# Optimization experiments

Measured on AMD Instinct MI355X. Metric: run time of the kernel, lower is better.

## Reference

```python
import jax, jax.numpy as jnp
import numpy as np

M, A, E, H = 2048, 64, 128, 256
NUM_BOND_TYPES, NUM_ATOM_TYPES = 4, 118

def setup_inputs() -> dict:
    key = jax.random.key(0)
    ks = jax.random.split(key, 12)
    s = 0.02
    return {
        'node_rep': jax.random.normal(ks[0], (M, A, H), jnp.float32),
        'edge_index': jax.random.randint(ks[1], (M, 2, E), 0, A, jnp.int32),
        'bond_type_target': jax.random.randint(ks[2], (M, E), 0, NUM_BOND_TYPES, jnp.int32),
        'atom_type_target': jax.random.randint(ks[3], (M, A), 0, NUM_ATOM_TYPES, jnp.int32),
        'Wp1': jax.random.normal(ks[4], (H, H), jnp.float32) * s, 'bp1': jnp.zeros((H,), jnp.float32),
        'Wp2': jax.random.normal(ks[5], (H, H), jnp.float32) * s, 'bp2': jnp.zeros((H,), jnp.float32),
        'Wb1': jax.random.normal(ks[6], (2 * H, H), jnp.float32) * s, 'bb1': jnp.zeros((H,), jnp.float32),
        'Wb2': jax.random.normal(ks[7], (H, NUM_BOND_TYPES), jnp.float32) * s, 'bb2': jnp.zeros((NUM_BOND_TYPES,), jnp.float32),
        'Wa1': jax.random.normal(ks[8], (H, H), jnp.float32) * s, 'ba1': jnp.zeros((H,), jnp.float32),
        'Wa2': jax.random.normal(ks[9], (H, NUM_ATOM_TYPES), jnp.float32) * s, 'ba2': jnp.zeros((NUM_ATOM_TYPES,), jnp.float32),
    }

def _mlp(x, W1, b1, W2, b2):
    return jnp.maximum(x @ W1 + b1, 0.0) @ W2 + b2

def reference(node_rep, edge_index, bond_type_target, atom_type_target,
              Wp1, bp1, Wp2, bp2, Wb1, bb1, Wb2, bb2, Wa1, ba1, Wa2, ba2):
    # bond_if_proj: per-atom 2-layer MLP (dropout=0 -> identity)  [M,A,H]
    proj = _mlp(node_rep, Wp1, bp1, Wp2, bp2)
    # gather bond endpoint reps: index_select over atoms per molecule  [M,E,H]
    start = jnp.take_along_axis(proj, edge_index[:, 0, :, None], axis=1)
    end = jnp.take_along_axis(proj, edge_index[:, 1, :, None], axis=1)
    bt_in = jnp.concatenate([start, end], axis=-1)            # [M,E,2H]
    bt_logits = _mlp(bt_in, Wb1, bb1, Wb2, bb2)               # [M,E,4]
    bt_logp = jax.nn.log_softmax(bt_logits, axis=-1)
    # per-molecule mean CE averaged over molecules == global mean (equal sizes)
    bond_type_loss = -jnp.mean(jnp.take_along_axis(bt_logp, bond_type_target[..., None], axis=-1))
    bond_type_acc = jnp.mean((jnp.argmax(bt_logits, axis=-1) == bond_type_target).astype(jnp.float32))
    # atom type classifier on raw node reps  [M,A,118]
    at_logits = _mlp(node_rep, Wa1, ba1, Wa2, ba2)
    at_logp = jax.nn.log_softmax(at_logits, axis=-1)
    atom_type_loss = -jnp.mean(jnp.take_along_axis(at_logp, atom_type_target[..., None], axis=-1))
    atom_type_acc = jnp.mean((jnp.argmax(at_logits, axis=-1) == atom_type_target).astype(jnp.float32))
    loss = 0.5 * bond_type_loss + 0.5 * atom_type_loss
    return loss, bond_type_acc, atom_type_acc
```

## Files before the change

kernel.cpp:

```cpp
#include <hip/hip_runtime.h>
#include <hip/hip_bf16.h>

typedef __bf16 bf16x8 __attribute__((ext_vector_type(8)));
typedef float f32x16 __attribute__((ext_vector_type(16)));

__device__ inline unsigned short f2bf(float f) {
  __hip_bfloat16 h = __float2bfloat16(f);
  return *reinterpret_cast<unsigned short*>(&h);
}
__device__ inline unsigned pack2bf(float a, float b) {
  return (unsigned)f2bf(a) | ((unsigned)f2bf(b) << 16);
}
__device__ inline uint2 pack4bf(float a, float b, float c, float d) {
  uint2 r; r.x = pack2bf(a, b); r.y = pack2bf(c, d); return r;
}
__device__ inline bf16x8 as_bf16x8(uint4 v) { return __builtin_bit_cast(bf16x8, v); }
__device__ inline float bitf(unsigned u) { return __builtin_bit_cast(float, u); }
__device__ inline f32x16 mfma16(bf16x8 a, bf16x8 b, f32x16 c) {
  return __builtin_amdgcn_mfma_f32_32x32x16_bf16(a, b, c, 0, 0, 0);
}

#define BR(XB, R, KK)                                                          \
  ((XB) + (((((R) * 32 + l31) << 9) + ((KK) << 5) + (h << 4)) ^ swz))

#define GEMMS(XB, WPTR)                                                        \
  {                                                                            \
    const unsigned char* wb_ = (const unsigned char*)(WPTR) +                  \
                               ((cw + l31) << 5) + (h << 4);                   \
    acc00 = zero; acc01 = zero; acc10 = zero; acc11 = zero;                    \
    bf16x8 pB0 = *(const bf16x8*)BR(XB, 0, 0);                                 \
    bf16x8 pB1 = *(const bf16x8*)BR(XB, 1, 0);                                 \
    uint4 pA0 = *(const uint4*)(wb_);                                          \
    uint4 pA1 = *(const uint4*)(wb_ + 1024);                                   \
    _Pragma("clang loop unroll(disable)")                                      \
    for (int kk = 0; kk < 16; kk += 2) {                                       \
      bf16x8 qB0 = *(const bf16x8*)BR(XB, 0, kk + 1);                          \
      bf16x8 qB1 = *(const bf16x8*)BR(XB, 1, kk + 1);                          \
      uint4 qA0 = *(const uint4*)(wb_ + ((kk + 1) << 13));                     \
      uint4 qA1 = *(const uint4*)(wb_ + ((kk + 1) << 13) + 1024);              \
      acc00 = mfma16(as_bf16x8(pA0), pB0, acc00);                              \
      acc10 = mfma16(as_bf16x8(pA1), pB0, acc10);                              \
      acc01 = mfma16(as_bf16x8(pA0), pB1, acc01);                              \
      acc11 = mfma16(as_bf16x8(pA1), pB1, acc11);                              \
      if (kk + 2 < 16) {                                                       \
        pB0 = *(const bf16x8*)BR(XB, 0, kk + 2);                               \
        pB1 = *(const bf16x8*)BR(XB, 1, kk + 2);                               \
        pA0 = *(const uint4*)(wb_ + ((kk + 2) << 13));                         \
        pA1 = *(const uint4*)(wb_ + ((kk + 2) << 13) + 1024);                  \
      }                                                                        \
      acc00 = mfma16(as_bf16x8(qA0), qB0, acc00);                              \
      acc10 = mfma16(as_bf16x8(qA1), qB0, acc10);                              \
      acc01 = mfma16(as_bf16x8(qA0), qB1, acc01);                              \
      acc11 = mfma16(as_bf16x8(qA1), qB1, acc11);                              \
    }                                                                          \
  }

#define WB22(DB, ACC, R, C, BIASPTR)                                           \
  _Pragma("unroll")                                                            \
  for (int g = 0; g < 4; ++g) {                                                \
    int xr_ = (R) * 32 + l31;                                                  \
    int col = cw + (C) * 32 + g * 8 + h * 4;                                   \
    float4 bb = *(const float4*)((BIASPTR) + col);                             \
    float v0_ = fmaxf(ACC[4 * g + 0] + bb.x, 0.f);                             \
    float v1_ = fmaxf(ACC[4 * g + 1] + bb.y, 0.f);                             \
    float v2_ = fmaxf(ACC[4 * g + 2] + bb.z, 0.f);                             \
    float v3_ = fmaxf(ACC[4 * g + 3] + bb.w, 0.f);                             \
    int off = ((xr_ << 9) + (col << 1)) ^ ((xr_ & 7) << 4);                    \
    *(uint2*)((DB) + off) = pack4bf(v0_, v1_, v2_, v3_);                       \
  }

#define WB22R(DB, ACC, R, C)                                                   \
  _Pragma("unroll")                                                            \
  for (int g = 0; g < 4; ++g) {                                                \
    int xr_ = (R) * 32 + l31;                                                  \
    int col = cw + (C) * 32 + g * 8 + h * 4;                                   \
    int off = ((xr_ << 9) + (col << 1)) ^ ((xr_ & 7) << 4);                    \
    *(uint2*)((DB) + off) = pack4bf(ACC[4 * g + 0], ACC[4 * g + 1],            \
                                    ACC[4 * g + 2], ACC[4 * g + 3]);           \
  }

#define STAGE_X(DST, SRC)                                                      \
  _Pragma("unroll")                                                            \
  for (int it = 0; it < 4; ++it) {                                             \
    int lb = (it * 512 + tid) * 16;                                            \
    int d_ = lb ^ (((lb >> 9) & 7) << 4);                                      \
    const float4* s4 = (const float4*)((SRC) + (lb >> 1));                     \
    float4 f0 = s4[0], f1 = s4[1];                                             \
    uint4 v_ = { pack2bf(f0.x, f0.y), pack2bf(f0.z, f0.w),                     \
                 pack2bf(f1.x, f1.y), pack2bf(f1.z, f1.w) };                   \
    *(uint4*)((DST) + d_) = v_;                                                \
  }

__global__ __launch_bounds__(256) void k_pack(
    const float* __restrict__ wp1, const float* __restrict__ wa1,
    const float* __restrict__ wa2,
    unsigned short* __restrict__ dp1, unsigned short* __restrict__ da1,
    unsigned short* __restrict__ da2, float* __restrict__ accum)
{
  int b = blockIdx.x, tid = threadIdx.x;
  if (b == 0 && tid < 8) accum[tid] = 0.f;
  const float* src; unsigned short* dst; int e, logN, Nreal;
  if (b < 256)       { src = wp1; dst = dp1; e = b * 256 + tid;          logN = 8; Nreal = 256; }
  else if (b < 512)  { src = wa1; dst = da1; e = (b - 256) * 256 + tid;  logN = 8; Nreal = 256; }
  else               { src = wa2; dst = da2; e = (b - 512) * 256 + tid;  logN = 7; Nreal = 118; }
  int dk = e & 15;
  int rest = e >> 4;
  int n = rest & ((1 << logN) - 1);
  int kk = rest >> logN;
  int k = kk * 16 + dk;
  float v = (n < Nreal) ? src[k * Nreal + n] : 0.f;
  dst[e] = f2bf(v);
}

__global__ __launch_bounds__(256) void k_fold(
    const float* __restrict__ wp2, const float* __restrict__ wb1,
    const float* __restrict__ bp2, const float* __restrict__ bb1,
    unsigned short* __restrict__ dct, unsigned short* __restrict__ dcb,
    float* __restrict__ bias_e)
{
  int b = blockIdx.x, n = threadIdx.x;
  if (b < 512) {
    int k = b & 255;
    int off = (b < 256) ? 0 : 256;
    float s = 0.f;
    for (int t = 0; t < 256; ++t)
      s += wp2[k * 256 + t] * wb1[(t + off) * 256 + n];
    unsigned short* dst = (b < 256) ? dct : dcb;
    dst[((k >> 4) * 256 + n) * 16 + (k & 15)] = f2bf(s);
  } else {
    float s = bb1[n];
    for (int t = 0; t < 256; ++t)
      s += bp2[t] * (wb1[t * 256 + n] + wb1[(256 + t) * 256 + n]);
    bias_e[n] = s;
  }
}

__global__ __launch_bounds__(512, 4) void k_mol(
    const float* __restrict__ node, const int* __restrict__ eidx,
    const int* __restrict__ btt, const int* __restrict__ att,
    const unsigned short* __restrict__ wp1p, const float* __restrict__ bp1,
    const unsigned short* __restrict__ wctp, const unsigned short* __restrict__ wcbp,
    const float* __restrict__ bias_e, const float* __restrict__ wb2,
    const float* __restrict__ bb2,
    const unsigned short* __restrict__ wa1p, const float* __restrict__ ba1,
    const unsigned short* __restrict__ wa2p, const float* __restrict__ ba2,
    float* __restrict__ accum)
{
  __shared__ __align__(16) unsigned char bufA[32768];
  __shared__ __align__(16) unsigned char bufB[32768];
  __shared__ float s_bias[256];
  __shared__ float4 s_wb2[256];
  __shared__ float s_b2a[128];
  __shared__ float s_red[16];
  const int tid = threadIdx.x;
  const int lane = tid & 63;
  const int w = tid >> 6;
  const int l31 = lane & 31;
  const int h = lane >> 5;
  const int swz = (l31 & 7) << 4;
  const int mat = w >> 2;
  const int cw = (w & 3) * 64;
  const int m = blockIdx.x;

  STAGE_X(bufA, node + (long)m * 16384);
  if (tid < 256) {
    s_bias[tid] = bias_e[tid];
    s_wb2[tid] = ((const float4*)wb2)[tid];
  }
  if (tid < 128) s_b2a[tid] = (tid < 118) ? ba2[tid] : 0.f;
  const int t_at = att[m * 64 + (tid >> 3)];
  __syncthreads();

  f32x16 zero = {};
  f32x16 acc00, acc01, acc10, acc11;

  GEMMS(bufA, mat ? wp1p : wa1p);
  if (mat == 0) {
    WB22(bufB, acc00, 0, 0, ba1);
    WB22(bufB, acc10, 0, 1, ba1);
    WB22(bufB, acc01, 1, 0, ba1);
    WB22(bufB, acc11, 1, 1, ba1);
  }
  __syncthreads();
  if (mat == 1) {
    WB22(bufA, acc00, 0, 0, bp1);
    WB22(bufA, acc10, 0, 1, bp1);
    WB22(bufA, acc01, 1, 0, bp1);
    WB22(bufA, acc11, 1, 1, bp1);
  }
  __syncthreads();

  f32x16 aL = zero;
  {
    const int cw2 = (w & 3) * 32;
    const int R2 = w >> 2;
    const unsigned char* wb_ = (const unsigned char*)wa2p +
                               ((cw2 + l31) << 5) + (h << 4);
    bf16x8 pB = *(const bf16x8*)BR(bufB, R2, 0);
    uint4 pA = *(const uint4*)(wb_);
    _Pragma("clang loop unroll(disable)")
    for (int kk = 0; kk < 16; kk += 2) {
      bf16x8 qB = *(const bf16x8*)BR(bufB, R2, kk + 1);
      uint4 qA = *(const uint4*)(wb_ + ((kk + 1) << 12));
      aL = mfma16(as_bf16x8(pA), pB, aL);
      if (kk + 2 < 16) {
        pB = *(const bf16x8*)BR(bufB, R2, kk + 2);
        pA = *(const uint4*)(wb_ + ((kk + 2) << 12));
      }
      aL = mfma16(as_bf16x8(qA), qB, aL);
    }
  }
  __syncthreads();

  {
    const int cw2 = (w & 3) * 32;
    const int r0 = (w >> 2) * 32 + l31;
    const int rx = (r0 & 7) << 4;
    #pragma unroll
    for (int g = 0; g < 4; ++g) {
      int colb = cw2 + 8 * g + 4 * h;
      uint4 val;
      val.x = __builtin_bit_cast(unsigned, aL[4 * g + 0] + s_b2a[colb + 0]);
      val.y = __builtin_bit_cast(unsigned, aL[4 * g + 1] + s_b2a[colb + 1]);
      val.z = __builtin_bit_cast(unsigned, aL[4 * g + 2] + s_b2a[colb + 2]);
      val.w = __builtin_bit_cast(unsigned, aL[4 * g + 3] + s_b2a[colb + 3]);
      *(uint4*)(bufB + (((r0 << 9) + (colb << 2)) ^ rx)) = val;
    }
  }
  __syncthreads();

  {
    const int row = tid >> 3, g8 = tid & 7;
    const unsigned char* lr = bufB + (row << 9);
    const int rx = (row & 7) << 4;
    float mx = -3.0e38f; int am = 127;
    #pragma unroll
    for (int j = 0; j < 4; ++j) {
      int ch = g8 + 8 * j;
      if (ch < 30) {
        float4 f = *(const float4*)(lr + (((ch << 4)) ^ rx));
        int c = ch * 4;
        if (f.x > mx) { mx = f.x; am = c; }
        if (f.y > mx) { mx = f.y; am = c + 1; }
        if (c + 2 < 118 && f.z > mx) { mx = f.z; am = c + 2; }
        if (c + 3 < 118 && f.w > mx) { mx = f.w; am = c + 3; }
      }
    }
    #pragma unroll
    for (int d = 1; d < 8; d <<= 1) {
      float mo = __shfl_xor(mx, d); int amo = __shfl_xor(am, d);
      if (mo > mx || (mo == mx && amo < am)) { mx = mo; am = amo; }
    }
    float s = 0.f, vt = 0.f;
    #pragma unroll
    for (int j = 0; j < 4; ++j) {
      int ch = g8 + 8 * j;
      if (ch < 30) {
        float4 f = *(const float4*)(lr + (((ch << 4)) ^ rx));
        int c = ch * 4;
        s += __expf(f.x - mx);
        s += __expf(f.y - mx);
        if (c + 2 < 118) s += __expf(f.z - mx);
        if (c + 3 < 118) s += __expf(f.w - mx);
        if (c == t_at) vt = f.x;
        if (c + 1 == t_at) vt = f.y;
        if (c + 2 == t_at) vt = f.z;
        if (c + 3 == t_at) vt = f.w;
      }
    }
    #pragma unroll
    for (int d = 1; d < 8; d <<= 1) { s += __shfl_xor(s, d); vt += __shfl_xor(vt, d); }
    float ce = 0.f, cc = 0.f;
    if (g8 == 0) { ce = __logf(s) + mx - vt; cc = (am == t_at) ? 1.f : 0.f; }
    #pragma unroll
    for (int d = 1; d < 64; d <<= 1) { ce += __shfl_xor(ce, d); cc += __shfl_xor(cc, d); }
    if (lane == 0) { s_red[w * 2] = ce; s_red[w * 2 + 1] = cc; }
  }

  GEMMS(bufA, mat ? wcbp : wctp);
  const int es = eidx[m * 256 + (tid >> 2)];
  const int ed = eidx[m * 256 + 128 + (tid >> 2)];
  const int etg = btt[m * 128 + (tid >> 2)];
  const float b20 = bb2[0], b21 = bb2[1], b22 = bb2[2], b23 = bb2[3];
  __syncthreads();
  if (tid == 0) {
    float sa = 0.f, sb = 0.f;
    #pragma unroll
    for (int i = 0; i < 8; ++i) { sa += s_red[2 * i]; sb += s_red[2 * i + 1]; }
    atomicAdd(accum + 2, sa);
    atomicAdd(accum + 3, sb);
  }
  if (mat == 0) {
    WB22R(bufA, acc00, 0, 0);
    WB22R(bufA, acc10, 0, 1);
    WB22R(bufA, acc01, 1, 0);
    WB22R(bufA, acc11, 1, 1);
  } else {
    WB22R(bufB, acc00, 0, 0);
    WB22R(bufB, acc10, 0, 1);
    WB22R(bufB, acc01, 1, 0);
    WB22R(bufB, acc11, 1, 1);
  }
  __syncthreads();

  {
    const int qf = tid & 3;
    float lg0 = 0.f, lg1 = 0.f, lg2 = 0.f, lg3 = 0.f;
    #pragma unroll
    for (int j = 0; j < 8; ++j) {
      int c0 = qf * 64 + j * 8;
      int offS = ((es << 9) + (c0 << 1)) ^ ((es & 7) << 4);
      int offD = ((ed << 9) + (c0 << 1)) ^ ((ed & 7) << 4);
      uint4 us = *(const uint4*)(bufA + offS);
      uint4 ud = *(const uint4*)(bufB + offD);
      const unsigned* pu = (const unsigned*)&us;
      const unsigned* pv = (const unsigned*)&ud;
      #pragma unroll
      for (int q = 0; q < 4; ++q) {
        unsigned ua = pu[q], ub = pv[q];
        int c = c0 + 2 * q;
        float hlo = bitf(ua << 16) + bitf(ub << 16) + s_bias[c];
        float hhi = bitf(ua & 0xffff0000u) + bitf(ub & 0xffff0000u) + s_bias[c + 1];
        hlo = fmaxf(hlo, 0.f); hhi = fmaxf(hhi, 0.f);
        float4 w0 = s_wb2[c], w1 = s_wb2[c + 1];
        lg0 = fmaf(hlo, w0.x, fmaf(hhi, w1.x, lg0));
        lg1 = fmaf(hlo, w0.y, fmaf(hhi, w1.y, lg1));
        lg2 = fmaf(hlo, w0.z, fmaf(hhi, w1.z, lg2));
        lg3 = fmaf(hlo, w0.w, fmaf(hhi, w1.w, lg3));
      }
    }
    lg0 += __shfl_xor(lg0, 1); lg1 += __shfl_xor(lg1, 1);
    lg2 += __shfl_xor(lg2, 1); lg3 += __shfl_xor(lg3, 1);
    lg0 += __shfl_xor(lg0, 2); lg1 += __shfl_xor(lg1, 2);
    lg2 += __shfl_xor(lg2, 2); lg3 += __shfl_xor(lg3, 2);
    float ce = 0.f, cc = 0.f;
    if (qf == 0) {
      float l0 = lg0 + b20, l1 = lg1 + b21, l2 = lg2 + b22, l3 = lg3 + b23;
      int t = etg;
      int am = 0; float mx = l0;
      if (l1 > mx) { mx = l1; am = 1; }
      if (l2 > mx) { mx = l2; am = 2; }
      if (l3 > mx) { mx = l3; am = 3; }
      float s = __expf(l0 - mx) + __expf(l1 - mx) + __expf(l2 - mx) + __expf(l3 - mx);
      float lt = (t == 0) ? l0 : (t == 1) ? l1 : (t == 2) ? l2 : l3;
      ce = __logf(s) + mx - lt;
      cc = (am == t) ? 1.f : 0.f;
    }
    #pragma unroll
    for (int d = 1; d < 64; d <<= 1) { ce += __shfl_xor(ce, d); cc += __shfl_xor(cc, d); }
    if (lane == 0) { s_red[w * 2] = ce; s_red[w * 2 + 1] = cc; }
    __syncthreads();
    if (tid == 0) {
      float sa = 0.f, sb = 0.f;
      #pragma unroll
      for (int i = 0; i < 8; ++i) { sa += s_red[2 * i]; sb += s_red[2 * i + 1]; }
      atomicAdd(accum + 0, sa);
      atomicAdd(accum + 1, sb);
    }
  }
}

__global__ __launch_bounds__(64) void k_final(const float* __restrict__ accum,
                                              float* __restrict__ out)
{
  if (threadIdx.x == 0) {
    float bce = accum[0] / 262144.f;
    float bcc = accum[1] / 262144.f;
    float ace = accum[2] / 131072.f;
    float acc_ = accum[3] / 131072.f;
    out[0] = 0.5f * bce + 0.5f * ace;
    out[1] = bcc;
    out[2] = acc_;
  }
}

extern "C" void kernel_launch(void* const* d_in, const int* in_sizes, int n_in,
                              void* d_out, int out_size, void* d_ws, size_t ws_size,
                              hipStream_t stream)
{
  const float* node = (const float*)d_in[0];
  const int* eidx   = (const int*)d_in[1];
  const int* btt    = (const int*)d_in[2];
  const int* att    = (const int*)d_in[3];
  const float* Wp1 = (const float*)d_in[4];
  const float* bp1 = (const float*)d_in[5];
  const float* Wp2 = (const float*)d_in[6];
  const float* bp2 = (const float*)d_in[7];
  const float* Wb1 = (const float*)d_in[8];
  const float* bb1 = (const float*)d_in[9];
  const float* Wb2 = (const float*)d_in[10];
  const float* bb2 = (const float*)d_in[11];
  const float* Wa1 = (const float*)d_in[12];
  const float* ba1 = (const float*)d_in[13];
  const float* Wa2 = (const float*)d_in[14];
  const float* ba2 = (const float*)d_in[15];

  char* ws = (char*)d_ws;
  float* accum = (float*)ws;
  unsigned short* dp1 = (unsigned short*)(ws + 256);
  unsigned short* da1 = (unsigned short*)(ws + 131328);
  unsigned short* da2 = (unsigned short*)(ws + 262400);
  unsigned short* dct = (unsigned short*)(ws + 327936);
  unsigned short* dcb = (unsigned short*)(ws + 459008);
  float* bias_e       = (float*)(ws + 590080);

  k_pack<<<640, 256, 0, stream>>>(Wp1, Wa1, Wa2, dp1, da1, da2, accum);
  k_fold<<<513, 256, 0, stream>>>(Wp2, Wb1, bp2, bb1, dct, dcb, bias_e);
  k_mol<<<2048, 512, 0, stream>>>(node, eidx, btt, att, dp1, bp1, dct, dcb,
                                  bias_e, Wb2, bb2, da1, ba1, da2, ba2, accum);
  k_final<<<1, 64, 0, stream>>>(accum, (float*)d_out);
}
```

Measured before the change: 200.0 us.

## Split fused molecule kernel into separate bond and atom kernels

The single per-molecule kernel, which ran the atom classifier and bond path together with 512 threads, is split into k_bond (512 threads) and k_atom (256 threads). Each kernel now re-reads and converts node_rep. The atom path computes log-softmax straight from MFMA accumulators with shuffle-based log-sum-exp merges instead of staging logits in shared memory. The bond path folds bias_e into the packed start projection so the edge loop skips a bias add. Per-wave atomics replace the block reduction through shared memory. In exchange it reads node_rep twice from global memory, adds a launch and issues more atomics, but uses less LDS in the atom kernel and fewer barriers.

```diff
diff --git a/kernel.cpp b/kernel.cpp
--- a/kernel.cpp
+++ b/kernel.cpp
@@ -55,34 +55,27 @@
     }                                                                          \
   }
 
-#define WB22(DB, ACC, R, C, BIASPTR)                                           \
+#define PACK1(ACC, G, CB, BIASPTR, RELU)                                       \
+  __extension__({                                                              \
+    float4 bb_ = *(const float4*)((BIASPTR) + (CB) + (G) * 8 + 4 * h);         \
+    float x0_ = ACC[4 * (G) + 0] + bb_.x, x1_ = ACC[4 * (G) + 1] + bb_.y,      \
+          x2_ = ACC[4 * (G) + 2] + bb_.z, x3_ = ACC[4 * (G) + 3] + bb_.w;      \
+    if (RELU) { x0_ = fmaxf(x0_, 0.f); x1_ = fmaxf(x1_, 0.f);                  \
+                x2_ = fmaxf(x2_, 0.f); x3_ = fmaxf(x3_, 0.f); }                \
+    pack4bf(x0_, x1_, x2_, x3_);                                               \
+  })
+#define PACK1R(ACC, G)                                                         \
+  pack4bf(ACC[4 * (G) + 0], ACC[4 * (G) + 1], ACC[4 * (G) + 2], ACC[4 * (G) + 3])
+
+#define WR1(DB, V, XR, CB, G)                                                  \
+  { int off_ = (((XR) << 9) + ((((CB) + (G) * 8 + 4 * h)) << 1)) ^             \
+               (((XR) & 7) << 4);                                              \
+    *(uint2*)((DB) + off_) = (V); }
+
+#define STAGE_X(DST, SRC, NT, ITERS)                                           \
   _Pragma("unroll")                                                            \
-  for (int g = 0; g < 4; ++g) {                                                \
-    int xr_ = (R) * 32 + l31;                                                  \
-    int col = cw + (C) * 32 + g * 8 + h * 4;                                   \
-    float4 bb = *(const float4*)((BIASPTR) + col);                             \
-    float v0_ = fmaxf(ACC[4 * g + 0] + bb.x, 0.f);                             \
-    float v1_ = fmaxf(ACC[4 * g + 1] + bb.y, 0.f);                             \
-    float v2_ = fmaxf(ACC[4 * g + 2] + bb.z, 0.f);                             \
-    float v3_ = fmaxf(ACC[4 * g + 3] + bb.w, 0.f);                             \
-    int off = ((xr_ << 9) + (col << 1)) ^ ((xr_ & 7) << 4);                    \
-    *(uint2*)((DB) + off) = pack4bf(v0_, v1_, v2_, v3_);                       \
-  }
-
-#define WB22R(DB, ACC, R, C)                                                   \
-  _Pragma("unroll")                                                            \
-  for (int g = 0; g < 4; ++g) {                                                \
-    int xr_ = (R) * 32 + l31;                                                  \
-    int col = cw + (C) * 32 + g * 8 + h * 4;                                   \
-    int off = ((xr_ << 9) + (col << 1)) ^ ((xr_ & 7) << 4);                    \
-    *(uint2*)((DB) + off) = pack4bf(ACC[4 * g + 0], ACC[4 * g + 1],            \
-                                    ACC[4 * g + 2], ACC[4 * g + 3]);           \
-  }
-
-#define STAGE_X(DST, SRC)                                                      \
-  _Pragma("unroll")                                                            \
-  for (int it = 0; it < 4; ++it) {                                             \
-    int lb = (it * 512 + tid) * 16;                                            \
+  for (int it = 0; it < (ITERS); ++it) {                                       \
+    int lb = (it * (NT) + tid) * 16;                                           \
     int d_ = lb ^ (((lb >> 9) & 7) << 4);                                      \
     const float4* s4 = (const float4*)((SRC) + (lb >> 1));                     \
     float4 f0 = s4[0], f1 = s4[1];                                             \
@@ -90,6 +83,15 @@
                  pack2bf(f1.x, f1.y), pack2bf(f1.z, f1.w) };                   \
     *(uint4*)((DST) + d_) = v_;                                                \
   }
+
+#define LSE_MERGE(MX, AM, S, VT, D)                                            \
+  { float omx_ = __shfl_xor(MX, D); int oam_ = __shfl_xor(AM, D);              \
+    float os_ = __shfl_xor(S, D); float ovt_ = __shfl_xor(VT, D);              \
+    float nmx_ = fmaxf(MX, omx_);                                              \
+    S = S * __expf(MX - nmx_) + os_ * __expf(omx_ - nmx_);                     \
+    VT += ovt_;                                                                \
+    if (omx_ > MX || (omx_ == MX && oam_ < AM)) AM = oam_;                     \
+    MX = nmx_; }
 
 __global__ __launch_bounds__(256) void k_pack(
     const float* __restrict__ wp1, const float* __restrict__ wa1,
@@ -135,171 +137,226 @@
   }
 }
 
-__global__ __launch_bounds__(512, 4) void k_mol(
-    const float* __restrict__ node, const int* __restrict__ eidx,
-    const int* __restrict__ btt, const int* __restrict__ att,
-    const unsigned short* __restrict__ wp1p, const float* __restrict__ bp1,
-    const unsigned short* __restrict__ wctp, const unsigned short* __restrict__ wcbp,
-    const float* __restrict__ bias_e, const float* __restrict__ wb2,
-    const float* __restrict__ bb2,
+__global__ __launch_bounds__(256, 4) void k_atom(
+    const float* __restrict__ node, const int* __restrict__ att,
     const unsigned short* __restrict__ wa1p, const float* __restrict__ ba1,
     const unsigned short* __restrict__ wa2p, const float* __restrict__ ba2,
     float* __restrict__ accum)
 {
   __shared__ __align__(16) unsigned char bufA[32768];
-  __shared__ __align__(16) unsigned char bufB[32768];
-  __shared__ float s_bias[256];
-  __shared__ float4 s_wb2[256];
-  __shared__ float s_b2a[128];
-  __shared__ float s_red[16];
+  __shared__ __align__(16) unsigned char part[4096];
   const int tid = threadIdx.x;
   const int lane = tid & 63;
   const int w = tid >> 6;
   const int l31 = lane & 31;
   const int h = lane >> 5;
   const int swz = (l31 & 7) << 4;
-  const int mat = w >> 2;
-  const int cw = (w & 3) * 64;
+  const int cw = w * 64;
   const int m = blockIdx.x;
 
-  STAGE_X(bufA, node + (long)m * 16384);
-  if (tid < 256) {
-    s_bias[tid] = bias_e[tid];
-    s_wb2[tid] = ((const float4*)wb2)[tid];
-  }
-  if (tid < 128) s_b2a[tid] = (tid < 118) ? ba2[tid] : 0.f;
-  const int t_at = att[m * 64 + (tid >> 3)];
+  STAGE_X(bufA, node + (long)m * 16384, 256, 8);
+  const int tA0 = att[m * 64 + l31];
+  const int tA1 = att[m * 64 + 32 + l31];
   __syncthreads();
 
   f32x16 zero = {};
   f32x16 acc00, acc01, acc10, acc11;
 
-  GEMMS(bufA, mat ? wp1p : wa1p);
-  if (mat == 0) {
-    WB22(bufB, acc00, 0, 0, ba1);
-    WB22(bufB, acc10, 0, 1, ba1);
-    WB22(bufB, acc01, 1, 0, ba1);
-    WB22(bufB, acc11, 1, 1, ba1);
-  }
-  __syncthreads();
-  if (mat == 1) {
-    WB22(bufA, acc00, 0, 0, bp1);
-    WB22(bufA, acc10, 0, 1, bp1);
-    WB22(bufA, acc01, 1, 0, bp1);
-    WB22(bufA, acc11, 1, 1, bp1);
-  }
-  __syncthreads();
-
-  f32x16 aL = zero;
+  GEMMS(bufA, wa1p);
+  uint2 q00 = PACK1(acc00, 0, cw, ba1, 1), q01 = PACK1(acc00, 1, cw, ba1, 1),
+        q02 = PACK1(acc00, 2, cw, ba1, 1), q03 = PACK1(acc00, 3, cw, ba1, 1);
+  uint2 q10 = PACK1(acc10, 0, cw + 32, ba1, 1), q11 = PACK1(acc10, 1, cw + 32, ba1, 1),
+        q12 = PACK1(acc10, 2, cw + 32, ba1, 1), q13 = PACK1(acc10, 3, cw + 32, ba1, 1);
+  uint2 q20 = PACK1(acc01, 0, cw, ba1, 1), q21 = PACK1(acc01, 1, cw, ba1, 1),
+        q22 = PACK1(acc01, 2, cw, ba1, 1), q23 = PACK1(acc01, 3, cw, ba1, 1);
+  uint2 q30 = PACK1(acc11, 0, cw + 32, ba1, 1), q31 = PACK1(acc11, 1, cw + 32, ba1, 1),
+        q32 = PACK1(acc11, 2, cw + 32, ba1, 1), q33 = PACK1(acc11, 3, cw + 32, ba1, 1);
+  __syncthreads();
+  WR1(bufA, q00, l31, cw, 0) WR1(bufA, q01, l31, cw, 1)
+  WR1(bufA, q02, l31, cw, 2) WR1(bufA, q03, l31, cw, 3)
+  WR1(bufA, q10, l31, cw + 32, 0) WR1(bufA, q11, l31, cw + 32, 1)
+  WR1(bufA, q12, l31, cw + 32, 2) WR1(bufA, q13, l31, cw + 32, 3)
+  WR1(bufA, q20, 32 + l31, cw, 0) WR1(bufA, q21, 32 + l31, cw, 1)
+  WR1(bufA, q22, 32 + l31, cw, 2) WR1(bufA, q23, 32 + l31, cw, 3)
+  WR1(bufA, q30, 32 + l31, cw + 32, 0) WR1(bufA, q31, 32 + l31, cw + 32, 1)
+  WR1(bufA, q32, 32 + l31, cw + 32, 2) WR1(bufA, q33, 32 + l31, cw + 32, 3)
+  __syncthreads();
+
+  const int cw2 = w * 32;
+  f32x16 aL0 = zero, aL1 = zero;
   {
-    const int cw2 = (w & 3) * 32;
-    const int R2 = w >> 2;
     const unsigned char* wb_ = (const unsigned char*)wa2p +
                                ((cw2 + l31) << 5) + (h << 4);
-    bf16x8 pB = *(const bf16x8*)BR(bufB, R2, 0);
+    bf16x8 pB0 = *(const bf16x8*)BR(bufA, 0, 0);
+    bf16x8 pB1 = *(const bf16x8*)BR(bufA, 1, 0);
     uint4 pA = *(const uint4*)(wb_);
     _Pragma("clang loop unroll(disable)")
     for (int kk = 0; kk < 16; kk += 2) {
-      bf16x8 qB = *(const bf16x8*)BR(bufB, R2, kk + 1);
+      bf16x8 qB0 = *(const bf16x8*)BR(bufA, 0, kk + 1);
+      bf16x8 qB1 = *(const bf16x8*)BR(bufA, 1, kk + 1);
       uint4 qA = *(const uint4*)(wb_ + ((kk + 1) << 12));
-      aL = mfma16(as_bf16x8(pA), pB, aL);
+      aL0 = mfma16(as_bf16x8(pA), pB0, aL0);
+      aL1 = mfma16(as_bf16x8(pA), pB1, aL1);
       if (kk + 2 < 16) {
-        pB = *(const bf16x8*)BR(bufB, R2, kk + 2);
+        pB0 = *(const bf16x8*)BR(bufA, 0, kk + 2);
+        pB1 = *(const bf16x8*)BR(bufA, 1, kk + 2);
         pA = *(const uint4*)(wb_ + ((kk + 2) << 12));
       }
-      aL = mfma16(as_bf16x8(qA), qB, aL);
-    }
+      aL0 = mfma16(as_bf16x8(qA), qB0, aL0);
+      aL1 = mfma16(as_bf16x8(qA), qB1, aL1);
+    }
+  }
+
+  float mx0 = -3.0e38f, s0 = 0.f, vt0 = 0.f; int am0 = 127;
+  float mx1 = -3.0e38f, s1 = 0.f, vt1 = 0.f; int am1 = 127;
+  #pragma unroll
+  for (int q = 0; q < 16; ++q) {
+    int c = cw2 + (q & 3) + 8 * (q >> 2) + 4 * h;
+    float bz = (c < 118) ? ba2[c] : 0.f;
+    float v0 = (c < 118) ? aL0[q] + bz : -3.0e38f;
+    float v1 = (c < 118) ? aL1[q] + bz : -3.0e38f;
+    aL0[q] = v0; aL1[q] = v1;
+    if (v0 > mx0) { mx0 = v0; am0 = c; }
+    if (v1 > mx1) { mx1 = v1; am1 = c; }
+  }
+  #pragma unroll
+  for (int q = 0; q < 16; ++q) {
+    int c = cw2 + (q & 3) + 8 * (q >> 2) + 4 * h;
+    if (c < 118) {
+      s0 += __expf(aL0[q] - mx0);
+      s1 += __expf(aL1[q] - mx1);
+      if (c == tA0) vt0 = aL0[q];
+      if (c == tA1) vt1 = aL1[q];
+    }
+  }
+  LSE_MERGE(mx0, am0, s0, vt0, 32)
+  LSE_MERGE(mx1, am1, s1, vt1, 32)
+  if (h == 0) {
+    float4 P0 = { mx0, (float)am0, s0, vt0 };
+    float4 P1 = { mx1, (float)am1, s1, vt1 };
+    *(float4*)(part + l31 * 64 + ((w ^ (l31 & 3)) << 4)) = P0;
+    *(float4*)(part + (32 + l31) * 64 + ((w ^ (l31 & 3)) << 4)) = P1;
   }
   __syncthreads();
 
   {
-    const int cw2 = (w & 3) * 32;
-    const int r0 = (w >> 2) * 32 + l31;
-    const int rx = (r0 & 7) << 4;
-    #pragma unroll
-    for (int g = 0; g < 4; ++g) {
-      int colb = cw2 + 8 * g + 4 * h;
-      uint4 val;
-      val.x = __builtin_bit_cast(unsigned, aL[4 * g + 0] + s_b2a[colb + 0]);
-      val.y = __builtin_bit_cast(unsigned, aL[4 * g + 1] + s_b2a[colb + 1]);
-      val.z = __builtin_bit_cast(unsigned, aL[4 * g + 2] + s_b2a[colb + 2]);
-      val.w = __builtin_bit_cast(unsigned, aL[4 * g + 3] + s_b2a[colb + 3]);
-      *(uint4*)(bufB + (((r0 << 9) + (colb << 2)) ^ rx)) = val;
-    }
-  }
-  __syncthreads();
-
-  {
-    const int row = tid >> 3, g8 = tid & 7;
-    const unsigned char* lr = bufB + (row << 9);
-    const int rx = (row & 7) << 4;
-    float mx = -3.0e38f; int am = 127;
-    #pragma unroll
-    for (int j = 0; j < 4; ++j) {
-      int ch = g8 + 8 * j;
-      if (ch < 30) {
-        float4 f = *(const float4*)(lr + (((ch << 4)) ^ rx));
-        int c = ch * 4;
-        if (f.x > mx) { mx = f.x; am = c; }
-        if (f.y > mx) { mx = f.y; am = c + 1; }
-        if (c + 2 < 118 && f.z > mx) { mx = f.z; am = c + 2; }
-        if (c + 3 < 118 && f.w > mx) { mx = f.w; am = c + 3; }
-      }
-    }
-    #pragma unroll
-    for (int d = 1; d < 8; d <<= 1) {
-      float mo = __shfl_xor(mx, d); int amo = __shfl_xor(am, d);
-      if (mo > mx || (mo == mx && amo < am)) { mx = mo; am = amo; }
-    }
-    float s = 0.f, vt = 0.f;
-    #pragma unroll
-    for (int j = 0; j < 4; ++j) {
-      int ch = g8 + 8 * j;
-      if (ch < 30) {
-        float4 f = *(const float4*)(lr + (((ch << 4)) ^ rx));
-        int c = ch * 4;
-        s += __expf(f.x - mx);
-        s += __expf(f.y - mx);
-        if (c + 2 < 118) s += __expf(f.z - mx);
-        if (c + 3 < 118) s += __expf(f.w - mx);
-        if (c == t_at) vt = f.x;
-        if (c + 1 == t_at) vt = f.y;
-        if (c + 2 == t_at) vt = f.z;
-        if (c + 3 == t_at) vt = f.w;
-      }
-    }
-    #pragma unroll
-    for (int d = 1; d < 8; d <<= 1) { s += __shfl_xor(s, d); vt += __shfl_xor(vt, d); }
+    const int row = tid >> 2, pw = tid & 3;
+    float4 p = *(const float4*)(part + row * 64 + ((pw ^ (row & 3)) << 4));
+    float mx = p.x, s = p.z, vt = p.w; int am = (int)p.y;
+    LSE_MERGE(mx, am, s, vt, 1)
+    LSE_MERGE(mx, am, s, vt, 2)
     float ce = 0.f, cc = 0.f;
-    if (g8 == 0) { ce = __logf(s) + mx - vt; cc = (am == t_at) ? 1.f : 0.f; }
+    if (pw == 0) {
+      int t = att[m * 64 + row];
+      ce = __logf(s) + mx - vt;
+      cc = (am == t) ? 1.f : 0.f;
+    }
     #pragma unroll
     for (int d = 1; d < 64; d <<= 1) { ce += __shfl_xor(ce, d); cc += __shfl_xor(cc, d); }
-    if (lane == 0) { s_red[w * 2] = ce; s_red[w * 2 + 1] = cc; }
-  }
-
+    if (lane == 0) { atomicAdd(accum + 2, ce); atomicAdd(accum + 3, cc); }
+  }
+}
+
+__global__ __launch_bounds__(512, 4) void k_bond(
+    const float* __restrict__ node, const int* __restrict__ eidx,
+    const int* __restrict__ btt,
+    const unsigned short* __restrict__ wp1p, const float* __restrict__ bp1,
+    const unsigned short* __restrict__ wctp, const unsigned short* __restrict__ wcbp,
+    const float* __restrict__ bias_e, const float* __restrict__ wb2,
+    const float* __restrict__ bb2, float* __restrict__ accum)
+{
+  __shared__ __align__(16) unsigned char bufA[32768];
+  __shared__ __align__(16) unsigned char bufB[32768];
+  __shared__ float4 s_wb2[256];
+  const int tid = threadIdx.x;
+  const int lane = tid & 63;
+  const int w = tid >> 6;
+  const int l31 = lane & 31;
+  const int h = lane >> 5;
+  const int swz = (l31 & 7) << 4;
+  const int m = blockIdx.x;
+
+  STAGE_X(bufA, node + (long)m * 16384, 512, 4);
+  if (tid < 256) s_wb2[tid] = ((const float4*)wb2)[tid];
+  __syncthreads();
+
+  f32x16 zero = {};
+
+  const int cw1 = w * 32;
+  f32x16 aR0 = zero, aR1 = zero;
+  {
+    const unsigned char* wb_ = (const unsigned char*)wp1p +
+                               ((cw1 + l31) << 5) + (h << 4);
+    bf16x8 pB0 = *(const bf16x8*)BR(bufA, 0, 0);
+    bf16x8 pB1 = *(const bf16x8*)BR(bufA, 1, 0);
+    uint4 pA = *(const uint4*)(wb_);
+    _Pragma("clang loop unroll(disable)")
+    for (int kk = 0; kk < 16; kk += 2) {
+      bf16x8 qB0 = *(const bf16x8*)BR(bufA, 0, kk + 1);
+      bf16x8 qB1 = *(const bf16x8*)BR(bufA, 1, kk + 1);
+      uint4 qA = *(const uint4*)(wb_ + ((kk + 1) << 13));
+      aR0 = mfma16(as_bf16x8(pA), pB0, aR0);
+      aR1 = mfma16(as_bf16x8(pA), pB1, aR1);
+      if (kk + 2 < 16) {
+        pB0 = *(const bf16x8*)BR(bufA, 0, kk + 2);
+        pB1 = *(const bf16x8*)BR(bufA, 1, kk + 2);
+        pA = *(const uint4*)(wb_ + ((kk + 2) << 13));
+      }
+      aR0 = mfma16(as_bf16x8(qA), qB0, aR0);
+      aR1 = mfma16(as_bf16x8(qA), qB1, aR1);
+    }
+  }
+  uint2 hb00 = PACK1(aR0, 0, cw1, bp1, 1), hb01 = PACK1(aR0, 1, cw1, bp1, 1),
+        hb02 = PACK1(aR0, 2, cw1, bp1, 1), hb03 = PACK1(aR0, 3, cw1, bp1, 1);
+  uint2 hb10 = PACK1(aR1, 0, cw1, bp1, 1), hb11 = PACK1(aR1, 1, cw1, bp1, 1),
+        hb12 = PACK1(aR1, 2, cw1, bp1, 1), hb13 = PACK1(aR1, 3, cw1, bp1, 1);
+  __syncthreads();
+  WR1(bufA, hb00, l31, cw1, 0) WR1(bufA, hb01, l31, cw1, 1)
+  WR1(bufA, hb02, l31, cw1, 2) WR1(bufA, hb03, l31, cw1, 3)
+  WR1(bufA, hb10, 32 + l31, cw1, 0) WR1(bufA, hb11, 32 + l31, cw1, 1)
+  WR1(bufA, hb12, 32 + l31, cw1, 2) WR1(bufA, hb13, 32 + l31, cw1, 3)
+  __syncthreads();
+
+  const int mat = w >> 2;
+  const int cw = (w & 3) * 64;
+  f32x16 acc00, acc01, acc10, acc11;
   GEMMS(bufA, mat ? wcbp : wctp);
+  uint2 q00, q01, q02, q03, q10, q11, q12, q13;
+  uint2 q20, q21, q22, q23, q30, q31, q32, q33;
+  if (mat == 0) {
+    q00 = PACK1(acc00, 0, cw, bias_e, 0); q01 = PACK1(acc00, 1, cw, bias_e, 0);
+    q02 = PACK1(acc00, 2, cw, bias_e, 0); q03 = PACK1(acc00, 3, cw, bias_e, 0);
+    q10 = PACK1(acc10, 0, cw + 32, bias_e, 0); q11 = PACK1(acc10, 1, cw + 32, bias_e, 0);
+    q12 = PACK1(acc10, 2, cw + 32, bias_e, 0); q13 = PACK1(acc10, 3, cw + 32, bias_e, 0);
+    q20 = PACK1(acc01, 0, cw, bias_e, 0); q21 = PACK1(acc01, 1, cw, bias_e, 0);
+    q22 = PACK1(acc01, 2, cw, bias_e, 0); q23 = PACK1(acc01, 3, cw, bias_e, 0);
+    q30 = PACK1(acc11, 0, cw + 32, bias_e, 0); q31 = PACK1(acc11, 1, cw + 32, bias_e, 0);
+    q32 = PACK1(acc11, 2, cw + 32, bias_e, 0); q33 = PACK1(acc11, 3, cw + 32, bias_e, 0);
+  } else {
+    q00 = PACK1R(acc00, 0); q01 = PACK1R(acc00, 1);
+    q02 = PACK1R(acc00, 2); q03 = PACK1R(acc00, 3);
+    q10 = PACK1R(acc10, 0); q11 = PACK1R(acc10, 1);
+    q12 = PACK1R(acc10, 2); q13 = PACK1R(acc10, 3);
+    q20 = PACK1R(acc01, 0); q21 = PACK1R(acc01, 1);
+    q22 = PACK1R(acc01, 2); q23 = PACK1R(acc01, 3);
+    q30 = PACK1R(acc11, 0); q31 = PACK1R(acc11, 1);
+    q32 = PACK1R(acc11, 2); q33 = PACK1R(acc11, 3);
+  }
   const int es = eidx[m * 256 + (tid >> 2)];
   const int ed = eidx[m * 256 + 128 + (tid >> 2)];
   const int etg = btt[m * 128 + (tid >> 2)];
   const float b20 = bb2[0], b21 = bb2[1], b22 = bb2[2], b23 = bb2[3];
   __syncthreads();
-  if (tid == 0) {
-    float sa = 0.f, sb = 0.f;
-    #pragma unroll
-    for (int i = 0; i < 8; ++i) { sa += s_red[2 * i]; sb += s_red[2 * i + 1]; }
-    atomicAdd(accum + 2, sa);
-    atomicAdd(accum + 3, sb);
-  }
-  if (mat == 0) {
-    WB22R(bufA, acc00, 0, 0);
-    WB22R(bufA, acc10, 0, 1);
-    WB22R(bufA, acc01, 1, 0);
-    WB22R(bufA, acc11, 1, 1);
-  } else {
-    WB22R(bufB, acc00, 0, 0);
-    WB22R(bufB, acc10, 0, 1);
-    WB22R(bufB, acc01, 1, 0);
-    WB22R(bufB, acc11, 1, 1);
+  {
+    unsigned char* db = mat ? bufB : bufA;
+    WR1(db, q00, l31, cw, 0) WR1(db, q01, l31, cw, 1)
+    WR1(db, q02, l31, cw, 2) WR1(db, q03, l31, cw, 3)
+    WR1(db, q10, l31, cw + 32, 0) WR1(db, q11, l31, cw + 32, 1)
+    WR1(db, q12, l31, cw + 32, 2) WR1(db, q13, l31, cw + 32, 3)
+    WR1(db, q20, 32 + l31, cw, 0) WR1(db, q21, 32 + l31, cw, 1)
+    WR1(db, q22, 32 + l31, cw, 2) WR1(db, q23, 32 + l31, cw, 3)
+    WR1(db, q30, 32 + l31, cw + 32, 0) WR1(db, q31, 32 + l31, cw + 32, 1)
+    WR1(db, q32, 32 + l31, cw + 32, 2) WR1(db, q33, 32 + l31, cw + 32, 3)
   }
   __syncthreads();
 
@@ -319,9 +376,8 @@
       for (int q = 0; q < 4; ++q) {
         unsigned ua = pu[q], ub = pv[q];
         int c = c0 + 2 * q;
-        float hlo = bitf(ua << 16) + bitf(ub << 16) + s_bias[c];
-        float hhi = bitf(ua & 0xffff0000u) + bitf(ub & 0xffff0000u) + s_bias[c + 1];
-        hlo = fmaxf(hlo, 0.f); hhi = fmaxf(hhi, 0.f);
+        float hlo = fmaxf(bitf(ua << 16) + bitf(ub << 16), 0.f);
+        float hhi = fmaxf(bitf(ua & 0xffff0000u) + bitf(ub & 0xffff0000u), 0.f);
         float4 w0 = s_wb2[c], w1 = s_wb2[c + 1];
         lg0 = fmaf(hlo, w0.x, fmaf(hhi, w1.x, lg0));
         lg1 = fmaf(hlo, w0.y, fmaf(hhi, w1.y, lg1));
@@ -348,15 +404,7 @@
     }
     #pragma unroll
     for (int d = 1; d < 64; d <<= 1) { ce += __shfl_xor(ce, d); cc += __shfl_xor(cc, d); }
-    if (lane == 0) { s_red[w * 2] = ce; s_red[w * 2 + 1] = cc; }
-    __syncthreads();
-    if (tid == 0) {
-      float sa = 0.f, sb = 0.f;
-      #pragma unroll
-      for (int i = 0; i < 8; ++i) { sa += s_red[2 * i]; sb += s_red[2 * i + 1]; }
-      atomicAdd(accum + 0, sa);
-      atomicAdd(accum + 1, sb);
-    }
+    if (lane == 0) { atomicAdd(accum + 0, ce); atomicAdd(accum + 1, cc); }
   }
 }
 
@@ -406,7 +454,8 @@
 
   k_pack<<<640, 256, 0, stream>>>(Wp1, Wa1, Wa2, dp1, da1, da2, accum);
   k_fold<<<513, 256, 0, stream>>>(Wp2, Wb1, bp2, bb1, dct, dcb, bias_e);
-  k_mol<<<2048, 512, 0, stream>>>(node, eidx, btt, att, dp1, bp1, dct, dcb,
-                                  bias_e, Wb2, bb2, da1, ba1, da2, ba2, accum);
+  k_bond<<<2048, 512, 0, stream>>>(node, eidx, btt, dp1, bp1, dct, dcb,
+                                   bias_e, Wb2, bb2, accum);
+  k_atom<<<2048, 256, 0, stream>>>(node, att, da1, ba1, da2, ba2, accum);
   k_final<<<1, 64, 0, stream>>>(accum, (float*)d_out);
 }
```

Result: slower. 701.0 us (+250.4%).
